# Performance work log

Hardware: AMD Instinct MI355X
Metric: run time of the kernel (lower is better)

The kernel has to match this reference:

```python
import jax, jax.numpy as jnp
import numpy as np


def setup_inputs() -> dict:
    key = jax.random.key(0)
    k1, k2, k3, k4 = jax.random.split(key, 4)
    B, N, D, d_dir = 2, 512, 512, 64
    scale_in = 1.0 / np.sqrt(D)
    scale_dir = 1.0 / np.sqrt(d_dir)
    t = jax.random.normal(k1, (B, N, D), dtype=jnp.float32)
    Wq = jax.random.normal(k2, (d_dir, D), dtype=jnp.float32) * scale_in
    Wk = jax.random.normal(k3, (d_dir, D), dtype=jnp.float32) * scale_in
    Wv = jax.random.normal(k4, (D, d_dir), dtype=jnp.float32) * scale_dir
    return {"t": t, "Wq": Wq, "Wk": Wk, "Wv": Wv}


def reference(t, Wq, Wk, Wv):
    # t: (B, N, D); Wq, Wk: (d_dir, D); Wv: (D, d_dir)
    q = jnp.einsum('bnd,ed->bne', t, Wq)  # (B, N, d_dir)
    k = jnp.einsum('bnd,ed->bne', t, Wk)  # (B, N, d_dir)
    had = q[:, :, None, :] * k[:, None, :, :]  # (B, N, N, d_dir)
    kappa = jnp.einsum('bije,de->bijd', had, Wv)  # (B, N, N, D)
    return kappa
```

## Files before the change

kernel.cpp:

```cpp
#include <hip/hip_runtime.h>
#include <hip/hip_bf16.h>

#define NB   512
#define DB   512
#define EB   64
#define JT   16
#define TPB  16

typedef __bf16 bf16x8 __attribute__((ext_vector_type(8)));
typedef float  f32x4  __attribute__((ext_vector_type(4)));

__global__ __launch_bounds__(64) void qk_proj_bf16(
    const float* __restrict__ t,
    const float* __restrict__ Wq,
    const float* __restrict__ Wk,
    __bf16* __restrict__ qb,
    __bf16* __restrict__ kb)
{
    __shared__ float trow[DB];
    const int bn = blockIdx.x;
    const int e  = threadIdx.x;
    #pragma unroll
    for (int idx = 0; idx < DB / 64; ++idx)
        trow[idx * 64 + e] = t[(size_t)bn * DB + idx * 64 + e];
    __syncthreads();

    float aq = 0.f, ak = 0.f;
    const float* wqr = Wq + (size_t)e * DB;
    const float* wkr = Wk + (size_t)e * DB;
    #pragma unroll 8
    for (int d = 0; d < DB; ++d) {
        const float tv = trow[d];
        aq += tv * wqr[d];
        ak += tv * wkr[d];
    }
    qb[bn * EB + e] = (__bf16)aq;
    kb[bn * EB + e] = (__bf16)ak;
}

__global__ void wv_to_bf16(const float* __restrict__ Wv, __bf16* __restrict__ wvb, int n)
{
    int i = blockIdx.x * blockDim.x + threadIdx.x;
    if (i < n) wvb[i] = (__bf16)Wv[i];
}

__global__ __launch_bounds__(256) void kappa_mfma(
    const __bf16* __restrict__ qb,
    const __bf16* __restrict__ kb,
    const __bf16* __restrict__ wvb,
    float* __restrict__ out)
{
    const int blk = blockIdx.x;
    const int bi  = blk >> 1;
    const int b   = bi >> 9;
    const int jt0 = (blk & 1) * TPB;
    const int w    = threadIdx.x >> 6;
    const int l    = threadIdx.x & 63;
    const int lrow = l & 15;
    const int lgrp = l >> 4;
    const int dbase = w * 128;

    __shared__ float lds[4 * JT * 128];
    float* __restrict__ wtile = lds + w * (JT * 128);

    const bf16x8 qv0 = *reinterpret_cast<const bf16x8*>(qb + (size_t)bi * EB + lgrp * 8);
    const bf16x8 qv1 = *reinterpret_cast<const bf16x8*>(qb + (size_t)bi * EB + 32 + lgrp * 8);

    bf16x8 bfrag[8][2];
    #pragma unroll
    for (int df = 0; df < 8; ++df) {
        const int d = dbase + df * 16 + lrow;
        #pragma unroll
        for (int ks = 0; ks < 2; ++ks) {
            const bf16x8 wv = *reinterpret_cast<const bf16x8*>(
                wvb + (size_t)d * EB + ks * 32 + lgrp * 8);
            const bf16x8 qq = ks ? qv1 : qv0;
            bf16x8 f;
            #pragma unroll
            for (int x = 0; x < 8; ++x)
                f[x] = (__bf16)((float)wv[x] * (float)qq[x]);
            bfrag[df][ks] = f;
        }
    }

    const __bf16* __restrict__ kbase = kb + (size_t)b * NB * EB;

    bf16x8 kv0 = *reinterpret_cast<const bf16x8*>(kbase + (size_t)(jt0 * JT + lrow) * EB + lgrp * 8);
    bf16x8 kv1 = *reinterpret_cast<const bf16x8*>(kbase + (size_t)(jt0 * JT + lrow) * EB + 32 + lgrp * 8);

    const int r_lo = l >> 5;
    const int cc   = l & 31;

    for (int t = 0; t < TPB; ++t) {
        f32x4 acc[8];
        #pragma unroll
        for (int df = 0; df < 8; ++df) {
            acc[df] = (f32x4){0.f, 0.f, 0.f, 0.f};
            acc[df] = __builtin_amdgcn_mfma_f32_16x16x32_bf16(bfrag[df][0], kv0, acc[df], 0, 0, 0);
            acc[df] = __builtin_amdgcn_mfma_f32_16x16x32_bf16(bfrag[df][1], kv1, acc[df], 0, 0, 0);
        }

        if (t + 1 < TPB) {
            const int jn = (jt0 + t + 1) * JT + lrow;
            kv0 = *reinterpret_cast<const bf16x8*>(kbase + (size_t)jn * EB + lgrp * 8);
            kv1 = *reinterpret_cast<const bf16x8*>(kbase + (size_t)jn * EB + 32 + lgrp * 8);
        }

        asm volatile("" ::: "memory");
        #pragma unroll
        for (int df = 0; df < 8; ++df) {
            const int sc = (df * 4 + lgrp) ^ (lrow & 7);
            *reinterpret_cast<f32x4*>(wtile + lrow * 128 + sc * 4) = acc[df];
        }
        asm volatile("" ::: "memory");

        float* __restrict__ obase =
            out + ((size_t)bi * NB + (size_t)(jt0 + t) * JT) * DB + dbase;
        #pragma unroll
        for (int p = 0; p < 8; ++p) {
            const int r  = 2 * p + r_lo;
            const int sc = cc ^ (r & 7);
            const f32x4 v = *reinterpret_cast<const f32x4*>(wtile + r * 128 + sc * 4);
            *reinterpret_cast<f32x4*>(obase + (size_t)r * DB + cc * 4) = v;
        }
    }
}

extern "C" void kernel_launch(void* const* d_in, const int* in_sizes, int n_in,
                              void* d_out, int out_size, void* d_ws, size_t ws_size,
                              hipStream_t stream) {
    const float* t  = (const float*)d_in[0];
    const float* Wq = (const float*)d_in[1];
    const float* Wk = (const float*)d_in[2];
    const float* Wv = (const float*)d_in[3];
    float* out = (float*)d_out;

    const int B = 2;

    __bf16* qb  = (__bf16*)d_ws;
    __bf16* kbf = qb + (size_t)B * NB * EB;
    __bf16* wvb = kbf + (size_t)B * NB * EB;

    qk_proj_bf16<<<dim3(B * NB), dim3(64), 0, stream>>>(t, Wq, Wk, qb, kbf);
    wv_to_bf16<<<dim3((DB * EB + 255) / 256), dim3(256), 0, stream>>>(Wv, wvb, DB * EB);

    kappa_mfma<<<dim3(2048), dim3(256), 0, stream>>>(qb, kbf, wvb, out);
}
```

Baseline: 234.5 us.

## Use persistent grid with strided tiles; fold q into k-side operand

The kappa kernel now launches 1024 persistent blocks, each walking 32 tiles strided by the grid so concurrently running blocks write contiguous output regions. The Wv fragments stay raw bf16 in registers, and the q*k Hadamard product is formed per step on the k-side operand instead of pre-scaling Wv by q. This aims to even out the write stream across the output and cut per-block setup. In exchange it adds a few multiplies per step and reloads q for every tile.

Result: slower. 242.2 us (+3.3%).

```diff
diff --git a/kernel.cpp b/kernel.cpp
--- a/kernel.cpp
+++ b/kernel.cpp
@@ -1,11 +1,12 @@
 #include <hip/hip_runtime.h>
 #include <hip/hip_bf16.h>
 
-#define NB   512
-#define DB   512
-#define EB   64
-#define JT   16
-#define TPB  16
+#define NB    512
+#define DB    512
+#define EB    64
+#define JT    16
+#define STEPS 32
+#define GRID  1024
 
 typedef __bf16 bf16x8 __attribute__((ext_vector_type(8)));
 typedef float  f32x4  __attribute__((ext_vector_type(4)));
@@ -50,10 +51,9 @@
     const __bf16* __restrict__ wvb,
     float* __restrict__ out)
 {
-    const int blk = blockIdx.x;
-    const int bi  = blk >> 1;
-    const int b   = bi >> 9;
-    const int jt0 = (blk & 1) * TPB;
+    const int bid = blockIdx.x;
+    const int jt  = bid & 31;
+    const int q0  = bid >> 5;
     const int w    = threadIdx.x >> 6;
     const int l    = threadIdx.x & 63;
     const int lrow = l & 15;
@@ -63,47 +63,51 @@
     __shared__ float lds[4 * JT * 128];
     float* __restrict__ wtile = lds + w * (JT * 128);
 
-    const bf16x8 qv0 = *reinterpret_cast<const bf16x8*>(qb + (size_t)bi * EB + lgrp * 8);
-    const bf16x8 qv1 = *reinterpret_cast<const bf16x8*>(qb + (size_t)bi * EB + 32 + lgrp * 8);
-
     bf16x8 bfrag[8][2];
     #pragma unroll
     for (int df = 0; df < 8; ++df) {
         const int d = dbase + df * 16 + lrow;
         #pragma unroll
-        for (int ks = 0; ks < 2; ++ks) {
-            const bf16x8 wv = *reinterpret_cast<const bf16x8*>(
+        for (int ks = 0; ks < 2; ++ks)
+            bfrag[df][ks] = *reinterpret_cast<const bf16x8*>(
                 wvb + (size_t)d * EB + ks * 32 + lgrp * 8);
-            const bf16x8 qq = ks ? qv1 : qv0;
-            bf16x8 f;
-            #pragma unroll
-            for (int x = 0; x < 8; ++x)
-                f[x] = (__bf16)((float)wv[x] * (float)qq[x]);
-            bfrag[df][ks] = f;
-        }
     }
 
-    const __bf16* __restrict__ kbase = kb + (size_t)b * NB * EB;
+    const int jrow = jt * JT + lrow;
 
-    bf16x8 kv0 = *reinterpret_cast<const bf16x8*>(kbase + (size_t)(jt0 * JT + lrow) * EB + lgrp * 8);
-    bf16x8 kv1 = *reinterpret_cast<const bf16x8*>(kbase + (size_t)(jt0 * JT + lrow) * EB + 32 + lgrp * 8);
+    int bi = q0;
+    bf16x8 qv0 = *reinterpret_cast<const bf16x8*>(qb + (size_t)bi * EB + lgrp * 8);
+    bf16x8 qv1 = *reinterpret_cast<const bf16x8*>(qb + (size_t)bi * EB + 32 + lgrp * 8);
+    bf16x8 kv0 = *reinterpret_cast<const bf16x8*>(kb + ((size_t)(bi >> 9) * NB + jrow) * EB + lgrp * 8);
+    bf16x8 kv1 = *reinterpret_cast<const bf16x8*>(kb + ((size_t)(bi >> 9) * NB + jrow) * EB + 32 + lgrp * 8);
 
     const int r_lo = l >> 5;
     const int cc   = l & 31;
 
-    for (int t = 0; t < TPB; ++t) {
+    for (int s = 0; s < STEPS; ++s) {
+        const int tile_id = s * GRID + bid;
+
+        bf16x8 a0, a1;
+        #pragma unroll
+        for (int x = 0; x < 8; ++x) {
+            a0[x] = (__bf16)((float)kv0[x] * (float)qv0[x]);
+            a1[x] = (__bf16)((float)kv1[x] * (float)qv1[x]);
+        }
+
         f32x4 acc[8];
         #pragma unroll
         for (int df = 0; df < 8; ++df) {
             acc[df] = (f32x4){0.f, 0.f, 0.f, 0.f};
-            acc[df] = __builtin_amdgcn_mfma_f32_16x16x32_bf16(bfrag[df][0], kv0, acc[df], 0, 0, 0);
-            acc[df] = __builtin_amdgcn_mfma_f32_16x16x32_bf16(bfrag[df][1], kv1, acc[df], 0, 0, 0);
+            acc[df] = __builtin_amdgcn_mfma_f32_16x16x32_bf16(bfrag[df][0], a0, acc[df], 0, 0, 0);
+            acc[df] = __builtin_amdgcn_mfma_f32_16x16x32_bf16(bfrag[df][1], a1, acc[df], 0, 0, 0);
         }
 
-        if (t + 1 < TPB) {
-            const int jn = (jt0 + t + 1) * JT + lrow;
-            kv0 = *reinterpret_cast<const bf16x8*>(kbase + (size_t)jn * EB + lgrp * 8);
-            kv1 = *reinterpret_cast<const bf16x8*>(kbase + (size_t)jn * EB + 32 + lgrp * 8);
+        if (s + 1 < STEPS) {
+            const int bin = (s + 1) * (GRID >> 5) + q0;
+            qv0 = *reinterpret_cast<const bf16x8*>(qb + (size_t)bin * EB + lgrp * 8);
+            qv1 = *reinterpret_cast<const bf16x8*>(qb + (size_t)bin * EB + 32 + lgrp * 8);
+            kv0 = *reinterpret_cast<const bf16x8*>(kb + ((size_t)(bin >> 9) * NB + jrow) * EB + lgrp * 8);
+            kv1 = *reinterpret_cast<const bf16x8*>(kb + ((size_t)(bin >> 9) * NB + jrow) * EB + 32 + lgrp * 8);
         }
 
         asm volatile("" ::: "memory");
@@ -114,8 +118,7 @@
         }
         asm volatile("" ::: "memory");
 
-        float* __restrict__ obase =
-            out + ((size_t)bi * NB + (size_t)(jt0 + t) * JT) * DB + dbase;
+        float* __restrict__ obase = out + (size_t)tile_id * (JT * DB) + dbase;
         #pragma unroll
         for (int p = 0; p < 8; ++p) {
             const int r  = 2 * p + r_lo;
@@ -144,5 +147,5 @@
     qk_proj_bf16<<<dim3(B * NB), dim3(64), 0, stream>>>(t, Wq, Wk, qb, kbf);
     wv_to_bf16<<<dim3((DB * EB + 255) / 256), dim3(256), 0, stream>>>(Wv, wvb, DB * EB);
 
-    kappa_mfma<<<dim3(2048), dim3(256), 0, stream>>>(qb, kbf, wvb, out);
+    kappa_mfma<<<dim3(GRID), dim3(256), 0, stream>>>(qb, kbf, wvb, out);
 }
```
